# Kernel tuning notes

Measured on AMD Instinct MI355X. Metric: run time of the kernel, lower is better.

The kernel has to match this reference:

```python
import jax, jax.numpy as jnp
import numpy as np

N = 100000
E = 1000000
F_IN = 64
HID = 128
NCLS = 32
G = 1024
EPS = 1e-5


def setup_inputs() -> dict:
    key = jax.random.key(0)
    ks = jax.random.split(key, 6)
    x = jax.random.normal(ks[0], (N, F_IN), dtype=jnp.float32)
    edge_index = jax.random.randint(ks[1], (2, E), 0, N, dtype=jnp.int64)
    batch = jnp.sort(jax.random.randint(ks[2], (N,), 0, G, dtype=jnp.int64))
    # parameters (init per _init_weights: uniform(-0.01,0.01) linears, BN w=0.1 b=0)
    W_gcn = jax.random.uniform(ks[3], (F_IN, HID), minval=-0.01, maxval=0.01, dtype=jnp.float32)
    b_gcn = jnp.zeros((HID,), jnp.float32)
    bn1_w = jnp.full((HID,), 0.1, jnp.float32)
    bn1_b = jnp.zeros((HID,), jnp.float32)
    W_out = jax.random.uniform(ks[4], (HID, NCLS), minval=-0.01, maxval=0.01, dtype=jnp.float32)
    b_out = jnp.zeros((NCLS,), jnp.float32)
    bn2_w = jnp.full((NCLS,), 0.1, jnp.float32)
    bn2_b = jnp.zeros((NCLS,), jnp.float32)
    return {"x": x, "edge_index": edge_index, "batch": batch,
            "W_gcn": W_gcn, "b_gcn": b_gcn, "bn1_w": bn1_w, "bn1_b": bn1_b,
            "W_out": W_out, "b_out": b_out, "bn2_w": bn2_w, "bn2_b": bn2_b}


def _batchnorm(h, w, b):
    # training-mode BN: biased batch statistics over dim 0
    mu = jnp.mean(h, axis=0)
    var = jnp.var(h, axis=0)
    return (h - mu) * jax.lax.rsqrt(var + EPS) * w + b


def reference(x, edge_index, batch, W_gcn, b_gcn, bn1_w, bn1_b, W_out, b_out, bn2_w, bn2_b):
    # --- GCNConv: add self loops, symmetric norm, transform, aggregate ---
    loop = jnp.arange(N, dtype=edge_index.dtype)
    src = jnp.concatenate([edge_index[0], loop])  # [E+N]
    dst = jnp.concatenate([edge_index[1], loop])
    deg = jax.ops.segment_sum(jnp.ones_like(dst, dtype=x.dtype), dst, num_segments=N)
    dinv = jax.lax.rsqrt(deg)  # deg >= 1 thanks to self loops
    coef = dinv[src] * dinv[dst]  # [E+N]
    h = x @ W_gcn  # [N, HID] transform before gather (as PyG)
    msg = h[src] * coef[:, None]  # [E+N, HID] gathered messages
    h = jax.ops.segment_sum(msg, dst, num_segments=N) + b_gcn
    # --- BN + ReLU (dropout is identity in eval) ---
    h = jax.nn.relu(_batchnorm(h, bn1_w, bn1_b))
    # --- global_mean_pool over graphs ---
    sums = jax.ops.segment_sum(h, batch, num_segments=G)  # [G, HID]
    cnt = jax.ops.segment_sum(jnp.ones((N,), h.dtype), batch, num_segments=G)
    pooled = sums / jnp.maximum(cnt, 1.0)[:, None]
    # --- head: Linear + BN ---
    out = pooled @ W_out + b_out
    return _batchnorm(out, bn2_w, bn2_b)
```

## Files before the change

kernel.cpp:

```cpp
#include <hip/hip_runtime.h>
#include <hip/hip_fp16.h>

constexpr int N    = 100000;
constexpr int E    = 1000000;
constexpr int FIN  = 64;
constexpr int HID  = 128;
constexpr int NCLS = 32;
constexpr int G    = 1024;
constexpr float EPS = 1e-5f;

constexpr int NTILE = (N + 127) / 128;

constexpr int NBUCK = 49;
constexpr int NPB   = 2048;
constexpr int EPB   = 2048;
constexpr int CAP   = 24576;
constexpr int BIN_GRID = (E + EPB - 1) / EPB;

typedef _Float16 half2v __attribute__((ext_vector_type(2)));

__device__ inline float fdot2f(__half2 a, __half2 b, float c) {
#if __has_builtin(__builtin_amdgcn_fdot2)
  return __builtin_amdgcn_fdot2(*(half2v*)&a, *(half2v*)&b, c, false);
#else
  float2 fa = __half22float2(a), fb = __half22float2(b);
  return c + fa.x * fb.x + fa.y * fb.y;
#endif
}

__global__ __launch_bounds__(256) void k_bin(const int* __restrict__ src,
                                             const int* __restrict__ dst,
                                             int* __restrict__ bucketCursor,
                                             uint2* __restrict__ bucketBuf) {
  __shared__ int bcnt[NBUCK];
  __shared__ int bscan[NBUCK];
  __shared__ int bdelta[NBUCK];
  __shared__ int lcur[NBUCK];
  __shared__ uint2 staged[EPB];
  int tid = threadIdx.x;
  int e0 = blockIdx.x * EPB;
  int cnt = E - e0 < EPB ? E - e0 : EPB;
  for (int i = tid; i < NBUCK; i += 256) bcnt[i] = 0;
  __syncthreads();
  for (int i = tid; i < cnt; i += 256) {
    int d = dst[e0 + i];
    atomicAdd(&bcnt[d >> 11], 1);
  }
  __syncthreads();
  if (tid == 0) {
    int run = 0;
    for (int b = 0; b < NBUCK; ++b) { bscan[b] = run; run += bcnt[b]; }
  }
  __syncthreads();
  if (tid < NBUCK) {
    int base = bcnt[tid] ? atomicAdd(&bucketCursor[tid], bcnt[tid]) : 0;
    bdelta[tid] = base - bscan[tid];
    lcur[tid]   = bscan[tid];
  }
  __syncthreads();
  for (int i = tid; i < cnt; i += 256) {
    int s = src[e0 + i], d = dst[e0 + i];
    int pos = atomicAdd(&lcur[d >> 11], 1);
    staged[pos] = make_uint2((unsigned)s, (unsigned)d);
  }
  __syncthreads();
  for (int i = tid; i < cnt; i += 256) {
    uint2 p = staged[i];
    int b = (int)(p.y >> 11);
    bucketBuf[(long long)b * CAP + bdelta[b] + i] = p;
  }
}

__global__ __launch_bounds__(1024) void k_build(const int* __restrict__ bucketLen,
                                                const uint2* __restrict__ bucketBuf,
                                                int* __restrict__ offsets,
                                                float* __restrict__ dinv,
                                                int* __restrict__ srclist) {
  __shared__ int cnt[NPB];
  __shared__ int part[1024];
  __shared__ int bbase;
  int b = blockIdx.x, tid = threadIdx.x;
  int n0 = b << 11;
  int nn = (N - n0 < NPB) ? (N - n0) : NPB;
  int len = bucketLen[b];
  cnt[tid] = 0; cnt[tid + 1024] = 0;
  __syncthreads();
  const uint2* buf = bucketBuf + (long long)b * CAP;
  for (int i = tid; i < len; i += 1024)
    atomicAdd(&cnt[(int)buf[i].y - n0], 1);
  if (tid == 0) {
    int s = 0;
    for (int j = 0; j < b; ++j) s += bucketLen[j];
    bbase = s;
  }
  __syncthreads();
  int c0 = cnt[2 * tid], c1 = cnt[2 * tid + 1];
  int psum = c0 + c1;
  part[tid] = psum;
  __syncthreads();
  for (int off = 1; off < 1024; off <<= 1) {
    int t = (tid >= off) ? part[tid - off] : 0;
    __syncthreads();
    part[tid] += t;
    __syncthreads();
  }
  int excl = part[tid] - psum;
  int base = bbase;
  int o0 = base + excl, o1 = base + excl + c0;
  __syncthreads();
  cnt[2 * tid] = o0; cnt[2 * tid + 1] = o1;
  if (2 * tid < nn) {
    offsets[n0 + 2 * tid] = o0;
    dinv[n0 + 2 * tid] = rsqrtf((float)c0 + 1.0f);
  }
  if (2 * tid + 1 < nn) {
    offsets[n0 + 2 * tid + 1] = o1;
    dinv[n0 + 2 * tid + 1] = rsqrtf((float)c1 + 1.0f);
  }
  if (b == NBUCK - 1 && tid == 1023) offsets[N] = base + part[1023];
  __syncthreads();
  for (int i = tid; i < len; i += 1024) {
    uint2 p = buf[i];
    int pos = atomicAdd(&cnt[(int)p.y - n0], 1);
    srclist[pos] = (int)p.x;
  }
}

__global__ void k_scale(const float4* __restrict__ x4, const float* __restrict__ dinv,
                        float2* __restrict__ y2) {
  int i = blockIdx.x * blockDim.x + threadIdx.x;
  if (i >= N * 16) return;
  int node = i >> 4;
  float c = dinv[node];
  float4 v = x4[i];
  union { float2 f; __half2 h[2]; } u;
  u.h[0] = __float22half2_rn(make_float2(v.x * c, v.y * c));
  u.h[1] = __float22half2_rn(make_float2(v.z * c, v.w * c));
  y2[i] = u.f;
}

__global__ void k_wprep(const float* __restrict__ W, __half2* __restrict__ w2g) {
  int idx = blockIdx.x * blockDim.x + threadIdx.x;
  if (idx >= 32 * 128) return;
  int kp = idx >> 7, col = idx & 127;
  w2g[idx] = __floats2half2_rn(W[(2 * kp) * 128 + col], W[(2 * kp + 1) * 128 + col]);
}

__global__ __launch_bounds__(256) void k_gather(const int* __restrict__ offsets,
                                                const int* __restrict__ srclist,
                                                const float* __restrict__ dinv,
                                                const float2* __restrict__ y2,
                                                float2* __restrict__ aggh) {
  int node = blockIdx.x * 16 + (threadIdx.x >> 4);
  int lane = threadIdx.x & 15;
  if (node >= N) return;
  int start = offsets[node], end = offsets[node + 1];
  float cd = dinv[node];

  union { float2 f; __half2 h[2]; } u;
  float4 a0, a1, a2, a3;
  u.f = y2[node * 16 + lane];
  {
    float2 f01 = __half22float2(u.h[0]);
    float2 f23 = __half22float2(u.h[1]);
    a0 = make_float4(f01.x, f01.y, f23.x, f23.y);
  }
  a1 = make_float4(0.f, 0.f, 0.f, 0.f);
  a2 = a1; a3 = a1;

  int i = start;
  for (; i + 3 < end; i += 4) {
    int s0 = srclist[i], s1 = srclist[i + 1], s2 = srclist[i + 2], s3 = srclist[i + 3];
    union { float2 f; __half2 h[2]; } u0, u1, u2, u3;
    u0.f = y2[(long long)s0 * 16 + lane];
    u1.f = y2[(long long)s1 * 16 + lane];
    u2.f = y2[(long long)s2 * 16 + lane];
    u3.f = y2[(long long)s3 * 16 + lane];
    float2 p, q;
    p = __half22float2(u0.h[0]); q = __half22float2(u0.h[1]);
    a0.x += p.x; a0.y += p.y; a0.z += q.x; a0.w += q.y;
    p = __half22float2(u1.h[0]); q = __half22float2(u1.h[1]);
    a1.x += p.x; a1.y += p.y; a1.z += q.x; a1.w += q.y;
    p = __half22float2(u2.h[0]); q = __half22float2(u2.h[1]);
    a2.x += p.x; a2.y += p.y; a2.z += q.x; a2.w += q.y;
    p = __half22float2(u3.h[0]); q = __half22float2(u3.h[1]);
    a3.x += p.x; a3.y += p.y; a3.z += q.x; a3.w += q.y;
  }
  for (; i < end; ++i) {
    int s = srclist[i];
    u.f = y2[(long long)s * 16 + lane];
    float2 p = __half22float2(u.h[0]);
    float2 q = __half22float2(u.h[1]);
    a0.x += p.x; a0.y += p.y; a0.z += q.x; a0.w += q.y;
  }
  float4 acc;
  acc.x = ((a0.x + a1.x) + (a2.x + a3.x)) * cd;
  acc.y = ((a0.y + a1.y) + (a2.y + a3.y)) * cd;
  acc.z = ((a0.z + a1.z) + (a2.z + a3.z)) * cd;
  acc.w = ((a0.w + a1.w) + (a2.w + a3.w)) * cd;
  union { float2 f; __half2 h[2]; } o;
  o.h[0] = __floats2half2_rn(acc.x, acc.y);
  o.h[1] = __floats2half2_rn(acc.z, acc.w);
  aggh[node * 16 + lane] = o.f;
}

__global__ __launch_bounds__(256) void k_gemm2h(const __half2* __restrict__ aggh2,
                                                const __half2* __restrict__ w2g,
                                                const float* __restrict__ b,
                                                __half2* __restrict__ h2,
                                                float* __restrict__ sums) {
  __shared__ __half2 Wl[32 * 128];
  __shared__ __half2 rowT[32 * 128];
  int tid  = threadIdx.x;
  int row0 = blockIdx.x * 128;
  {
    const float4* srcv = (const float4*)w2g;
    float4* dstv = (float4*)Wl;
    for (int i = tid; i < 1024; i += 256) dstv[i] = srcv[i];
  }
  {
    int half = tid >> 7;
    int r = tid & 127;
    int grow = row0 + r;
#pragma unroll
    for (int c = 0; c < 4; ++c) {
      int kp0 = half * 16 + c * 4;
      float4 v = make_float4(0.f, 0.f, 0.f, 0.f);
      if (grow < N) v = *(const float4*)&aggh2[(long long)grow * 32 + kp0];
      __half2* pv = (__half2*)&v;
      rowT[(kp0 + 0) * 128 + r] = pv[0];
      rowT[(kp0 + 1) * 128 + r] = pv[1];
      rowT[(kp0 + 2) * 128 + r] = pv[2];
      rowT[(kp0 + 3) * 128 + r] = pv[3];
    }
  }
  __syncthreads();

  int rt = tid >> 4, ct = tid & 15;
  float acc[8][8];
#pragma unroll
  for (int m = 0; m < 8; ++m)
#pragma unroll
    for (int j = 0; j < 8; ++j) acc[m][j] = 0.f;

#pragma unroll 2
  for (int kp = 0; kp < 32; ++kp) {
    float4 wv0 = *(const float4*)&Wl[kp * 128 + ct * 8];
    float4 wv1 = *(const float4*)&Wl[kp * 128 + ct * 8 + 4];
    float4 rv0 = *(const float4*)&rowT[kp * 128 + rt * 8];
    float4 rv1 = *(const float4*)&rowT[kp * 128 + rt * 8 + 4];
    __half2 wv[8], rv[8];
    *(float4*)&wv[0] = wv0; *(float4*)&wv[4] = wv1;
    *(float4*)&rv[0] = rv0; *(float4*)&rv[4] = rv1;
#pragma unroll
    for (int m = 0; m < 8; ++m)
#pragma unroll
      for (int j = 0; j < 8; ++j) acc[m][j] = fdot2f(rv[m], wv[j], acc[m][j]);
  }

  int cbase = ct * 8;
  float4 b0 = *(const float4*)&b[cbase];
  float4 b1 = *(const float4*)&b[cbase + 4];
  float bias[8] = {b0.x, b0.y, b0.z, b0.w, b1.x, b1.y, b1.z, b1.w};
  float s[8], s2[8];
#pragma unroll
  for (int j = 0; j < 8; ++j) { s[j] = 0.f; s2[j] = 0.f; }
#pragma unroll
  for (int m = 0; m < 8; ++m) {
    int grow = row0 + rt * 8 + m;
    if (grow < N) {
      float hv[8];
#pragma unroll
      for (int j = 0; j < 8; ++j) {
        hv[j] = acc[m][j] + bias[j];
        s[j] += hv[j];
        s2[j] += hv[j] * hv[j];
      }
      union { float4 f; __half2 h[4]; } o;
      o.h[0] = __floats2half2_rn(hv[0], hv[1]);
      o.h[1] = __floats2half2_rn(hv[2], hv[3]);
      o.h[2] = __floats2half2_rn(hv[4], hv[5]);
      o.h[3] = __floats2half2_rn(hv[6], hv[7]);
      *(float4*)&h2[(long long)grow * 64 + ct * 4] = o.f;
    }
  }
  __syncthreads();
  float* red = (float*)Wl;
#pragma unroll
  for (int j = 0; j < 8; ++j) {
    red[rt * 256 + cbase + j]       = s[j];
    red[rt * 256 + 128 + cbase + j] = s2[j];
  }
  __syncthreads();
  float tot = 0.f;
#pragma unroll 4
  for (int r = 0; r < 16; ++r) tot += red[r * 256 + tid];
  atomicAdd(&sums[tid], tot);
}

__global__ __launch_bounds__(128) void k_bn1_final(const float* __restrict__ sums,
                                                   const float* __restrict__ w,
                                                   const float* __restrict__ bb,
                                                   float* __restrict__ ss) {
  int tid = threadIdx.x;
  float mu  = sums[tid] * (1.0f / N);
  float var = sums[tid + 128] * (1.0f / N) - mu * mu;
  float rs  = rsqrtf(var + EPS);
  float sc  = rs * w[tid];
  ss[tid]       = sc;
  ss[tid + 128] = bb[tid] - mu * sc;
}

__global__ __launch_bounds__(256) void k_pool(const __half2* __restrict__ h2,
                                              const float* __restrict__ ss,
                                              const int* __restrict__ batch,
                                              float* __restrict__ pooled) {
  int g = blockIdx.x;
  int lo = 0, hi = N;
  while (lo < hi) { int m = (lo + hi) >> 1; if (batch[m] < g) lo = m + 1; else hi = m; }
  int lo2 = lo, hi2 = N;
  while (lo2 < hi2) { int m = (lo2 + hi2) >> 1; if (batch[m] < g + 1) lo2 = m + 1; else hi2 = m; }
  int start = lo, end = lo2;
  int tid = threadIdx.x;
  int cp = tid & 63, rp = tid >> 6;
  float sc0 = ss[2 * cp], sc1 = ss[2 * cp + 1];
  float sh0 = ss[2 * cp + 128], sh1 = ss[2 * cp + 129];
  float s0 = 0.f, s1 = 0.f;
  for (int r = start + rp; r < end; r += 4) {
    float2 f = __half22float2(h2[(long long)r * 64 + cp]);
    s0 += fmaxf(f.x * sc0 + sh0, 0.f);
    s1 += fmaxf(f.y * sc1 + sh1, 0.f);
  }
  __shared__ float red0[256], red1[256];
  red0[tid] = s0; red1[tid] = s1;
  __syncthreads();
  if (tid < 64) {
#pragma unroll
    for (int q = 1; q < 4; ++q) { s0 += red0[tid + q * 64]; s1 += red1[tid + q * 64]; }
    float cnt = fmaxf((float)(end - start), 1.0f);
    float2 o = make_float2(s0 / cnt, s1 / cnt);
    *(float2*)&pooled[g * 128 + 2 * tid] = o;
  }
}

__global__ __launch_bounds__(256) void k_head(const float* __restrict__ pooled,
                                              const float* __restrict__ W,
                                              const float* __restrict__ b,
                                              float* __restrict__ outpre,
                                              float* __restrict__ sums2) {
  int idx = blockIdx.x * 256 + threadIdx.x;
  int g = idx >> 5, c = idx & 31;
  float acc = b[c];
  const float* pr = pooled + g * 128;
#pragma unroll
  for (int k = 0; k < 128; ++k) acc += pr[k] * W[k * 32 + c];
  outpre[idx] = acc;
  __shared__ float red[256], red2[256];
  int tid = threadIdx.x;
  red[tid] = acc; red2[tid] = acc * acc;
  __syncthreads();
  for (int off = 128; off >= 32; off >>= 1) {
    if (tid < off) { red[tid] += red[tid + off]; red2[tid] += red2[tid + off]; }
    __syncthreads();
  }
  if (tid < 32) {
    atomicAdd(&sums2[tid], red[tid]);
    atomicAdd(&sums2[tid + 32], red2[tid]);
  }
}

__global__ void k_bn2f(const float* __restrict__ sums2, const float* __restrict__ w,
                       const float* __restrict__ b, float* __restrict__ ss2) {
  int c = threadIdx.x;
  float mu  = sums2[c] * (1.0f / G);
  float var = sums2[c + 32] * (1.0f / G) - mu * mu;
  float rs  = rsqrtf(var + EPS);
  float sc  = rs * w[c];
  ss2[c]      = sc;
  ss2[c + 32] = b[c] - mu * sc;
}

__global__ void k_bn2apply(const float* __restrict__ outpre, const float* __restrict__ ss2,
                           float* __restrict__ out) {
  int idx = blockIdx.x * 256 + threadIdx.x;
  int c = idx & 31;
  out[idx] = outpre[idx] * ss2[c] + ss2[c + 32];
}

extern "C" void kernel_launch(void* const* d_in, const int* in_sizes, int n_in,
                              void* d_out, int out_size, void* d_ws, size_t ws_size,
                              hipStream_t stream) {
  const float* x   = (const float*)d_in[0];
  const int* ei    = (const int*)d_in[1];
  const int* batch = (const int*)d_in[2];
  const float* Wg  = (const float*)d_in[3];
  const float* bg  = (const float*)d_in[4];
  const float* w1  = (const float*)d_in[5];
  const float* b1  = (const float*)d_in[6];
  const float* Wo  = (const float*)d_in[7];
  const float* bo  = (const float*)d_in[8];
  const float* w2  = (const float*)d_in[9];
  const float* b2  = (const float*)d_in[10];

  float* ws     = (float*)d_ws;
  float* dinv   = ws;
  float* aggh_f = ws + 100352;
  float* h2_f   = aggh_f + 1600512;
  float* ss     = h2_f + 6400000;
  float* sums   = ss + 256;
  float* sums2  = sums + 256;
  float* ss2    = sums2 + 64;
  float* pooled = ss2 + 64;
  float* outpre = pooled + G * 128;
  int* offsets  = (int*)(outpre + G * 32);
  int* srclist  = offsets + 100416;
  int* bucketCursor = srclist + E;
  __half2* w2g  = (__half2*)(bucketCursor + 64);
  uint2* bucketBuf = (uint2*)h2_f;
  float2* y2       = (float2*)(h2_f + 3100000);

  const int* src = ei;
  const int* dst = ei + E;

  hipMemsetAsync(bucketCursor, 0, 64 * sizeof(int), stream);
  hipMemsetAsync(sums, 0, (256 + 64) * sizeof(float), stream);
  k_wprep<<<16, 256, 0, stream>>>(Wg, w2g);
  k_bin<<<BIN_GRID, 256, 0, stream>>>(src, dst, bucketCursor, bucketBuf);
  k_build<<<NBUCK, 1024, 0, stream>>>(bucketCursor, bucketBuf, offsets, dinv, srclist);
  k_scale<<<(N * 16 + 255) / 256, 256, 0, stream>>>((const float4*)x, dinv, y2);
  k_gather<<<(N + 15) / 16, 256, 0, stream>>>(offsets, srclist, dinv, y2, (float2*)aggh_f);
  k_gemm2h<<<NTILE, 256, 0, stream>>>((const __half2*)aggh_f, w2g, bg,
                                      (__half2*)h2_f, sums);
  k_bn1_final<<<1, 128, 0, stream>>>(sums, w1, b1, ss);
  k_pool<<<G, 256, 0, stream>>>((const __half2*)h2_f, ss, batch, pooled);
  k_head<<<128, 256, 0, stream>>>(pooled, Wo, bo, outpre, sums2);
  k_bn2f<<<1, 32, 0, stream>>>(sums2, w2, b2, ss2);
  k_bn2apply<<<128, 256, 0, stream>>>(outpre, ss2, (float*)d_out);
}
```

Baseline: 228.7 us.

## Double bucket count for CSR build, parallelize scans, fold memsets into prep kernel

Splits the destination-bucketed CSR construction into 98 buckets of 1024 nodes, so k_build runs twice as many blocks with one node per thread, and k_bin processes 4096 edges per block. The serial per-block bucket scans in k_bin and k_build become parallel shared-memory Hillis-Steele scans. The two hipMemsetAsync calls are replaced by zeroing inside k_wprep, removing two launches. The cost is more atomics contention per bucket in k_bin and more scan barriers, and each bucket's capacity of 12288 edges is tighter against the expected average of about 10240.

```diff
diff --git a/kernel.cpp b/kernel.cpp
--- a/kernel.cpp
+++ b/kernel.cpp
@@ -11,10 +11,10 @@
 
 constexpr int NTILE = (N + 127) / 128;
 
-constexpr int NBUCK = 49;
-constexpr int NPB   = 2048;
-constexpr int EPB   = 2048;
-constexpr int CAP   = 24576;
+constexpr int NBUCK = 98;
+constexpr int NPB   = 1024;
+constexpr int EPB   = 4096;
+constexpr int CAP   = 12288;
 constexpr int BIN_GRID = (E + EPB - 1) / EPB;
 
 typedef _Float16 half2v __attribute__((ext_vector_type(2)));
@@ -33,9 +33,9 @@
                                              int* __restrict__ bucketCursor,
                                              uint2* __restrict__ bucketBuf) {
   __shared__ int bcnt[NBUCK];
-  __shared__ int bscan[NBUCK];
   __shared__ int bdelta[NBUCK];
   __shared__ int lcur[NBUCK];
+  __shared__ int part[128];
   __shared__ uint2 staged[EPB];
   int tid = threadIdx.x;
   int e0 = blockIdx.x * EPB;
@@ -44,29 +44,34 @@
   __syncthreads();
   for (int i = tid; i < cnt; i += 256) {
     int d = dst[e0 + i];
-    atomicAdd(&bcnt[d >> 11], 1);
-  }
-  __syncthreads();
-  if (tid == 0) {
-    int run = 0;
-    for (int b = 0; b < NBUCK; ++b) { bscan[b] = run; run += bcnt[b]; }
-  }
-  __syncthreads();
+    atomicAdd(&bcnt[d >> 10], 1);
+  }
+  __syncthreads();
+  if (tid < 128) part[tid] = (tid < NBUCK) ? bcnt[tid] : 0;
+  __syncthreads();
+  for (int off = 1; off < 128; off <<= 1) {
+    int t = 0;
+    if (tid < 128 && tid >= off) t = part[tid - off];
+    __syncthreads();
+    if (tid < 128) part[tid] += t;
+    __syncthreads();
+  }
   if (tid < NBUCK) {
+    int excl = part[tid] - bcnt[tid];
     int base = bcnt[tid] ? atomicAdd(&bucketCursor[tid], bcnt[tid]) : 0;
-    bdelta[tid] = base - bscan[tid];
-    lcur[tid]   = bscan[tid];
+    bdelta[tid] = base - excl;
+    lcur[tid]   = excl;
   }
   __syncthreads();
   for (int i = tid; i < cnt; i += 256) {
     int s = src[e0 + i], d = dst[e0 + i];
-    int pos = atomicAdd(&lcur[d >> 11], 1);
+    int pos = atomicAdd(&lcur[d >> 10], 1);
     staged[pos] = make_uint2((unsigned)s, (unsigned)d);
   }
   __syncthreads();
   for (int i = tid; i < cnt; i += 256) {
     uint2 p = staged[i];
-    int b = (int)(p.y >> 11);
+    int b = (int)(p.y >> 10);
     bucketBuf[(long long)b * CAP + bdelta[b] + i] = p;
   }
 }
@@ -78,25 +83,29 @@
                                                 int* __restrict__ srclist) {
   __shared__ int cnt[NPB];
   __shared__ int part[1024];
-  __shared__ int bbase;
+  __shared__ int sh_bbase;
   int b = blockIdx.x, tid = threadIdx.x;
-  int n0 = b << 11;
+  int n0 = b << 10;
   int nn = (N - n0 < NPB) ? (N - n0) : NPB;
   int len = bucketLen[b];
-  cnt[tid] = 0; cnt[tid + 1024] = 0;
+  cnt[tid] = 0;
+  if (tid < 128) part[tid] = (tid < NBUCK) ? bucketLen[tid] : 0;
+  __syncthreads();
+  for (int off = 1; off < 128; off <<= 1) {
+    int t = 0;
+    if (tid < 128 && tid >= off) t = part[tid - off];
+    __syncthreads();
+    if (tid < 128) part[tid] += t;
+    __syncthreads();
+  }
+  if (tid == b) sh_bbase = part[b] - len;
   __syncthreads();
   const uint2* buf = bucketBuf + (long long)b * CAP;
   for (int i = tid; i < len; i += 1024)
     atomicAdd(&cnt[(int)buf[i].y - n0], 1);
-  if (tid == 0) {
-    int s = 0;
-    for (int j = 0; j < b; ++j) s += bucketLen[j];
-    bbase = s;
-  }
-  __syncthreads();
-  int c0 = cnt[2 * tid], c1 = cnt[2 * tid + 1];
-  int psum = c0 + c1;
-  part[tid] = psum;
+  __syncthreads();
+  int v = cnt[tid];
+  part[tid] = v;
   __syncthreads();
   for (int off = 1; off < 1024; off <<= 1) {
     int t = (tid >= off) ? part[tid - off] : 0;
@@ -104,18 +113,13 @@
     part[tid] += t;
     __syncthreads();
   }
-  int excl = part[tid] - psum;
-  int base = bbase;
-  int o0 = base + excl, o1 = base + excl + c0;
-  __syncthreads();
-  cnt[2 * tid] = o0; cnt[2 * tid + 1] = o1;
-  if (2 * tid < nn) {
-    offsets[n0 + 2 * tid] = o0;
-    dinv[n0 + 2 * tid] = rsqrtf((float)c0 + 1.0f);
-  }
-  if (2 * tid + 1 < nn) {
-    offsets[n0 + 2 * tid + 1] = o1;
-    dinv[n0 + 2 * tid + 1] = rsqrtf((float)c1 + 1.0f);
+  int base = sh_bbase;
+  int o = base + part[tid] - v;
+  __syncthreads();
+  cnt[tid] = o;
+  if (tid < nn) {
+    offsets[n0 + tid] = o;
+    dinv[n0 + tid] = rsqrtf((float)v + 1.0f);
   }
   if (b == NBUCK - 1 && tid == 1023) offsets[N] = base + part[1023];
   __syncthreads();
@@ -139,8 +143,14 @@
   y2[i] = u.f;
 }
 
-__global__ void k_wprep(const float* __restrict__ W, __half2* __restrict__ w2g) {
+__global__ void k_wprep(const float* __restrict__ W, __half2* __restrict__ w2g,
+                        int* __restrict__ bucketCursor, float* __restrict__ sums) {
   int idx = blockIdx.x * blockDim.x + threadIdx.x;
+  if (blockIdx.x == 0 && threadIdx.x < 128) bucketCursor[threadIdx.x] = 0;
+  if (blockIdx.x == 1 && threadIdx.x < 64) {
+    float* p = sums + threadIdx.x;
+    p[0] = 0.f; p[64] = 0.f; p[128] = 0.f; p[192] = 0.f; p[256] = 0.f;
+  }
   if (idx >= 32 * 128) return;
   int kp = idx >> 7, col = idx & 127;
   w2g[idx] = __floats2half2_rn(W[(2 * kp) * 128 + col], W[(2 * kp + 1) * 128 + col]);
@@ -415,16 +425,14 @@
   int* offsets  = (int*)(outpre + G * 32);
   int* srclist  = offsets + 100416;
   int* bucketCursor = srclist + E;
-  __half2* w2g  = (__half2*)(bucketCursor + 64);
+  __half2* w2g  = (__half2*)(bucketCursor + 128);
   uint2* bucketBuf = (uint2*)h2_f;
   float2* y2       = (float2*)(h2_f + 3100000);
 
   const int* src = ei;
   const int* dst = ei + E;
 
-  hipMemsetAsync(bucketCursor, 0, 64 * sizeof(int), stream);
-  hipMemsetAsync(sums, 0, (256 + 64) * sizeof(float), stream);
-  k_wprep<<<16, 256, 0, stream>>>(Wg, w2g);
+  k_wprep<<<16, 256, 0, stream>>>(Wg, w2g, bucketCursor, sums);
   k_bin<<<BIN_GRID, 256, 0, stream>>>(src, dst, bucketCursor, bucketBuf);
   k_build<<<NBUCK, 1024, 0, stream>>>(bucketCursor, bucketBuf, offsets, dinv, srclist);
   k_scale<<<(N * 16 + 255) / 256, 256, 0, stream>>>((const float4*)x, dinv, y2);
```

Result: faster. 217.9 us (-4.7%).
